# Performance work log

Measured on AMD Instinct MI355X. Metric: run time of the kernel, lower is better.

Reference implementation:

```python
import jax, jax.numpy as jnp
import numpy as np

B, S, D = 4, 2048, 512
QKD = 256
HID = 3 * D  # expansion_factor=3
EPS = 1e-5


def _ln(x, g, b):
    m = jnp.mean(x, axis=-1, keepdims=True)
    v = jnp.mean((x - m) ** 2, axis=-1, keepdims=True)
    return (x - m) * jax.lax.rsqrt(v + EPS) * g + b


def setup_inputs() -> dict:
    key = jax.random.key(0)
    ks = jax.random.split(key, 12)
    s = lambda fan: 1.0 / np.sqrt(fan)
    return {
        "x":  jax.random.normal(ks[0], (B, S, D), jnp.float32),
        "Wm": jax.random.uniform(ks[1], (D, D), jnp.float32, -s(D), s(D)),
        "bm": jnp.zeros((D,), jnp.float32),
        "g1": jnp.ones((D,), jnp.float32),
        "b1": jnp.zeros((D,), jnp.float32),
        "Wh": jax.random.uniform(ks[2], (2 * HID, D), jnp.float32, -s(D), s(D)),
        "bh": jnp.zeros((2 * HID,), jnp.float32),
        "Wq": jax.random.uniform(ks[3], (QKD, D), jnp.float32, -s(D), s(D)),
        "bq": jnp.zeros((QKD,), jnp.float32),
        "Wb": jax.random.normal(ks[4], (QKD, QKD), jnp.float32),
        "Wo": jax.random.uniform(ks[5], (D, HID), jnp.float32, -s(HID), s(HID)),
        "bo": jnp.zeros((D,), jnp.float32),
        "g2": jnp.ones((D,), jnp.float32),
        "b2": jnp.zeros((D,), jnp.float32),
    }


def reference(x, Wm, bm, g1, b1, Wh, bh, Wq, bq, Wb, Wo, bo, g2, b2):
    seq_len = x.shape[-2]
    memory = jnp.einsum('bsd,ed->bse', x, Wm) + bm
    normed = _ln(x + memory, g1, b1)
    h = jax.nn.relu(jnp.einsum('bsd,hd->bsh', normed, Wh) + bh)
    v, gate = h[..., :HID], h[..., HID:]
    Z = jax.nn.relu(jnp.einsum('bsd,qd->bsq', normed, Wq) + bq)  # [B,S,QKD]
    QK = jnp.einsum('bid,de,bje->bij', Z, Wb, Z) / seq_len
    A = jax.nn.relu(QK) ** 2  # relu^2 attention, no softmax
    V = jnp.einsum('bij,bjd->bid', A, v) * gate
    out = _ln(jnp.einsum('bsh,dh->bsd', V, Wo) + bo, g2, b2)
    return out + x
```

## Files before the change

kernel.cpp:

```cpp
#include <hip/hip_runtime.h>

typedef unsigned short u16;
typedef unsigned char u8;
typedef __attribute__((ext_vector_type(8))) short short8;
typedef __attribute__((ext_vector_type(4))) float f32x4;
typedef __attribute__((ext_vector_type(8))) int int8v;
typedef __attribute__((ext_vector_type(4))) int int4v;

#define LN_EPS 1e-5f
#define SCALE_A 4096.f
#define SCALE_V 8.f
#define INV_SCALE_AV (1.f/32768.f)
#define SCALE_NRM 4.f
#define SCALE_WH 512.f
#define INV_SCALE_H (1.f/2048.f)
#define MX_ONE 0x7F7F7F7Fu

__device__ __forceinline__ u16 f2bf(float f){
    union { float f; unsigned u; } c; c.f = f;
    unsigned u = c.u + 0x7FFFu + ((c.u >> 16) & 1u);
    return (u16)(u >> 16);
}
__device__ __forceinline__ float bf2f(u16 h){
    union { unsigned u; float f; } c; c.u = ((unsigned)h) << 16;
    return c.f;
}
__device__ __forceinline__ u8 f2fp8(float f){
    int r = __builtin_amdgcn_cvt_pk_fp8_f32(f, 0.f, 0, false);
    return (u8)(r & 0xFF);
}
__device__ __forceinline__ u16 f2fp8x2(float a, float b){
    int r = __builtin_amdgcn_cvt_pk_fp8_f32(a, b, 0, false);
    return (u16)(r & 0xFFFF);
}

enum { EPI_NONE=0, EPI_BIAS_RES, EPI_BIAS_RELU, EPI_RELUSQ };
enum { OT_F32=0, OT_BF16=1, OT_FP8=2 };

__device__ __forceinline__ void gl2lds16(const void* g, void* lds){
    __builtin_amdgcn_global_load_lds(
        (const __attribute__((address_space(1))) unsigned*)g,
        (__attribute__((address_space(3))) unsigned*)lds, 16, 0, 0);
}

template<int EPI, int OT>
__global__ __launch_bounds__(256)
void mgemm(const u16* __restrict__ A, const u16* __restrict__ B, void* __restrict__ Cv,
           int K, int lda, int ldb, int ldc,
           long sAb, long sBb, long sCb,
           const float* __restrict__ bias,
           const float* __restrict__ ext, int ldext,
           float scale)
{
    __shared__ u16 sA[4096];
    __shared__ u16 sB[4096];
    const int tid = threadIdx.x;
    const int m0 = blockIdx.y * 128, n0 = blockIdx.x * 128;
    const int z  = blockIdx.z;
    const u16* Az = A + (size_t)z * sAb;
    const u16* Bz = B + (size_t)z * sBb;

    const int lane = tid & 63, quad = lane >> 4, l15 = lane & 15;
    const int wave = tid >> 6;
    const int wm = (wave >> 1) * 64, wn = (wave & 1) * 64;

    const u16* gA[2]; const u16* gB[2]; int lo[2];
#pragma unroll
    for (int r = 0; r < 2; r++){
        const int c = tid + r * 256;
        gA[r] = Az + (size_t)(m0 + (c & 127)) * lda + (c >> 7) * 8;
        gB[r] = Bz + (size_t)(n0 + (c & 127)) * ldb + (c >> 7) * 8;
        lo[r] = ((tid & 192) + r * 256) * 16;
    }

    f32x4 acc[4][4];
#pragma unroll
    for (int i = 0; i < 4; i++)
#pragma unroll
        for (int j = 0; j < 4; j++) acc[i][j] = (f32x4){0.f,0.f,0.f,0.f};

    const u16* fA = sA + quad * 1024 + (wm + l15) * 8;
    const u16* fB = sB + quad * 1024 + (wn + l15) * 8;

    for (int k0 = 0; k0 < K; k0 += 32){
#pragma unroll
        for (int r = 0; r < 2; r++){
            gl2lds16(gA[r] + k0, (char*)sA + lo[r]);
            gl2lds16(gB[r] + k0, (char*)sB + lo[r]);
        }
        __syncthreads();
        short8 a[4], b[4];
#pragma unroll
        for (int t = 0; t < 4; t++){
            a[t] = *(const short8*)(fA + t * 128);
            b[t] = *(const short8*)(fB + t * 128);
        }
#pragma unroll
        for (int i = 0; i < 4; i++)
#pragma unroll
            for (int j = 0; j < 4; j++)
                acc[i][j] = __builtin_amdgcn_mfma_f32_16x16x32_bf16(a[i], b[j], acc[i][j], 0, 0, 0);
        __syncthreads();
    }

    float* Cf = (float*)Cv; u16* Ch = (u16*)Cv; u8* C8 = (u8*)Cv;
    const size_t zc = (size_t)z * sCb;
#pragma unroll
    for (int i = 0; i < 4; i++){
#pragma unroll
        for (int j = 0; j < 4; j++){
            const int n = n0 + wn + j * 16 + l15;
            float bs = (EPI==EPI_BIAS_RES || EPI==EPI_BIAS_RELU) ? bias[n] : 0.f;
#pragma unroll
            for (int r = 0; r < 4; r++){
                const int m = m0 + wm + i * 16 + quad * 4 + r;
                float v = acc[i][j][r] + bs;
                if (EPI==EPI_BIAS_RES)
                    v += ext[(size_t)m * ldext + n];
                if (EPI==EPI_BIAS_RELU)
                    v = fmaxf(v, 0.f);
                if (EPI==EPI_RELUSQ){ float t = fmaxf(v * scale, 0.f); v = t * t * SCALE_A; }
                if (OT==OT_FP8)       C8[zc + (size_t)m * ldc + n] = f2fp8(v);
                else if (OT==OT_BF16) Ch[zc + (size_t)m * ldc + n] = f2bf(v);
                else                  Cf[zc + (size_t)m * ldc + n] = v;
            }
        }
    }
}

__global__ __launch_bounds__(256)
void mgemm_dual(const u16* __restrict__ Anrm, const u16* __restrict__ Whg,
                const u16* __restrict__ Wq,
                const float* __restrict__ bhg, const float* __restrict__ bq,
                u16* __restrict__ gbf, u16* __restrict__ Zb)
{
    __shared__ u16 sA[4096];
    __shared__ u16 sB[4096];
    const int tid = threadIdx.x;
    const bool isZ = blockIdx.x >= 12;
    const u16* Bm = isZ ? Wq : Whg;
    const float* bias = isZ ? bq : bhg;
    const int m0 = blockIdx.y * 128;
    const int n0 = (isZ ? (blockIdx.x - 12) : blockIdx.x) * 128;
    const int K = 512, lda = 512, ldb = 512;

    const int lane = tid & 63, quad = lane >> 4, l15 = lane & 15;
    const int wave = tid >> 6;
    const int wm = (wave >> 1) * 64, wn = (wave & 1) * 64;

    const u16* gA[2]; const u16* gB[2]; int lo[2];
#pragma unroll
    for (int r = 0; r < 2; r++){
        const int c = tid + r * 256;
        gA[r] = Anrm + (size_t)(m0 + (c & 127)) * lda + (c >> 7) * 8;
        gB[r] = Bm   + (size_t)(n0 + (c & 127)) * ldb + (c >> 7) * 8;
        lo[r] = ((tid & 192) + r * 256) * 16;
    }

    f32x4 acc[4][4];
#pragma unroll
    for (int i = 0; i < 4; i++)
#pragma unroll
        for (int j = 0; j < 4; j++) acc[i][j] = (f32x4){0.f,0.f,0.f,0.f};

    const u16* fA = sA + quad * 1024 + (wm + l15) * 8;
    const u16* fB = sB + quad * 1024 + (wn + l15) * 8;

    for (int k0 = 0; k0 < K; k0 += 32){
#pragma unroll
        for (int r = 0; r < 2; r++){
            gl2lds16(gA[r] + k0, (char*)sA + lo[r]);
            gl2lds16(gB[r] + k0, (char*)sB + lo[r]);
        }
        __syncthreads();
        short8 a[4], b[4];
#pragma unroll
        for (int t = 0; t < 4; t++){
            a[t] = *(const short8*)(fA + t * 128);
            b[t] = *(const short8*)(fB + t * 128);
        }
#pragma unroll
        for (int i = 0; i < 4; i++)
#pragma unroll
            for (int j = 0; j < 4; j++)
                acc[i][j] = __builtin_amdgcn_mfma_f32_16x16x32_bf16(a[i], b[j], acc[i][j], 0, 0, 0);
        __syncthreads();
    }

#pragma unroll
    for (int i = 0; i < 4; i++){
#pragma unroll
        for (int j = 0; j < 4; j++){
            const int n = n0 + wn + j * 16 + l15;
            const float bs = bias[n];
#pragma unroll
            for (int r = 0; r < 4; r++){
                const int m = m0 + wm + i * 16 + quad * 4 + r;
                float v = fmaxf(acc[i][j][r] + bs, 0.f);
                if (isZ) Zb[(size_t)m * 256 + n] = f2bf(v);
                else     gbf[(size_t)m * 1536 + n] = f2bf(v);
            }
        }
    }
}

template<bool VOUT>
__global__ __launch_bounds__(256)
void mgemm8mx(const u8* __restrict__ A, const u8* __restrict__ B, u16* __restrict__ C,
              int K, int lda, int ldb, int ldc,
              long sAb, long sBb, long sCb,
              const u16* __restrict__ gate, int ldext, long sEb,
              const float* __restrict__ bias, u8* __restrict__ vout)
{
    __shared__ u8 sA[16384];
    __shared__ u8 sB[16384];
    const int tid = threadIdx.x;
    const int m0 = blockIdx.y * 128, n0 = blockIdx.x * 128;
    const int z  = blockIdx.z;
    const u8* Az = A + (size_t)z * sAb;
    const u8* Bz = B + (size_t)z * sBb;

    const int lane = tid & 63, quad = lane >> 4, l15 = lane & 15;
    const int wave = tid >> 6;
    const int wm = (wave >> 1) * 64, wn = (wave & 1) * 64;

    const u8* gA[4]; const u8* gB[4]; int lo[4];
#pragma unroll
    for (int p = 0; p < 4; p++){
        const int r = p * 32 + (tid >> 3);
        const int j = (tid & 7) ^ (r & 7);
        gA[p] = Az + (size_t)(m0 + r) * lda + j * 16;
        gB[p] = Bz + (size_t)(n0 + r) * ldb + j * 16;
        lo[p] = p * 4096 + wave * 1024;
    }

    f32x4 acc[4][4];
#pragma unroll
    for (int i = 0; i < 4; i++)
#pragma unroll
        for (int j = 0; j < 4; j++) acc[i][j] = (f32x4){0.f,0.f,0.f,0.f};

    for (int k0 = 0; k0 < K; k0 += 128){
#pragma unroll
        for (int p = 0; p < 4; p++){
            gl2lds16(gA[p] + k0, (char*)sA + lo[p]);
            gl2lds16(gB[p] + k0, (char*)sB + lo[p]);
        }
        __syncthreads();
        int8v a[4], b[4];
#pragma unroll
        for (int i = 0; i < 4; i++){
            const int m = wm + i * 16 + l15;
            const int4v a0 = *(const int4v*)(sA + m * 128 + ((2*quad    ) ^ (m & 7)) * 16);
            const int4v a1 = *(const int4v*)(sA + m * 128 + ((2*quad + 1) ^ (m & 7)) * 16);
            a[i] = (int8v){a0[0],a0[1],a0[2],a0[3],a1[0],a1[1],a1[2],a1[3]};
            const int n = wn + i * 16 + l15;
            const int4v b0 = *(const int4v*)(sB + n * 128 + ((2*quad    ) ^ (n & 7)) * 16);
            const int4v b1 = *(const int4v*)(sB + n * 128 + ((2*quad + 1) ^ (n & 7)) * 16);
            b[i] = (int8v){b0[0],b0[1],b0[2],b0[3],b1[0],b1[1],b1[2],b1[3]};
        }
#pragma unroll
        for (int i = 0; i < 4; i++)
#pragma unroll
            for (int j = 0; j < 4; j++)
                acc[i][j] = __builtin_amdgcn_mfma_scale_f32_16x16x128_f8f6f4(
                    a[i], b[j], acc[i][j], 0, 0, 0, MX_ONE, 0, MX_ONE);
        __syncthreads();
    }

    const size_t zc = (size_t)z * sCb;
#pragma unroll
    for (int i = 0; i < 4; i++){
#pragma unroll
        for (int j = 0; j < 4; j++){
            const int n = n0 + wn + j * 16 + l15;
#pragma unroll
            for (int r = 0; r < 4; r++){
                const int m = m0 + wm + i * 16 + quad * 4 + r;
                if (VOUT){
                    float h = fmaxf(acc[i][j][r] * INV_SCALE_H + bias[n], 0.f);
                    vout[(size_t)m * 1536 + n] = f2fp8(h * SCALE_V);
                } else {
                    float v = acc[i][j][r] * INV_SCALE_AV
                            * bf2f(gate[(size_t)z * sEb + (size_t)m * ldext + n]);
                    C[zc + (size_t)m * ldc + n] = f2bf(v);
                }
            }
        }
    }
}

__global__ __launch_bounds__(256)
void ln1_k(const float* __restrict__ in, const float* __restrict__ g,
           const float* __restrict__ b, u16* __restrict__ nbf, u16* __restrict__ n8)
{
    const int row = blockIdx.x, tid = threadIdx.x;
    const size_t base = (size_t)row * 512 + tid * 2;
    const float2 v = *(const float2*)(in + base);
    float s = v.x + v.y, ss = v.x * v.x + v.y * v.y;
#pragma unroll
    for (int off = 32; off > 0; off >>= 1){
        s  += __shfl_down(s,  off);
        ss += __shfl_down(ss, off);
    }
    __shared__ float sbuf[8], ssbuf[8];
    const int wid = tid >> 6, lane = tid & 63;
    if (lane == 0){ sbuf[wid] = s; ssbuf[wid] = ss; }
    __syncthreads();
    if (tid == 0){
        float S = 0.f, SS = 0.f;
#pragma unroll
        for (int i = 0; i < 4; i++){ S += sbuf[i]; SS += ssbuf[i]; }
        const float mean = S * (1.f/512.f);
        const float var  = SS * (1.f/512.f) - mean * mean;
        sbuf[4]  = mean;
        ssbuf[4] = rsqrtf(var + LN_EPS);
    }
    __syncthreads();
    const float mean = sbuf[4], rstd = ssbuf[4];
    const float2 gg = *(const float2*)(g + tid * 2);
    const float2 bb = *(const float2*)(b + tid * 2);
    const float ox = (v.x - mean) * rstd * gg.x + bb.x;
    const float oy = (v.y - mean) * rstd * gg.y + bb.y;
    ((unsigned*)nbf)[(size_t)row * 256 + tid] =
        ((unsigned)f2bf(oy) << 16) | (unsigned)f2bf(ox);
    n8[(size_t)row * 256 + tid] = f2fp8x2(ox * SCALE_NRM, oy * SCALE_NRM);
}

__global__ __launch_bounds__(256)
void ln2_k(const u16* __restrict__ pa, long pstride,
           const float* __restrict__ bias2,
           const float* __restrict__ g, const float* __restrict__ b,
           const float* __restrict__ x, float* __restrict__ out)
{
    const int row = blockIdx.x, tid = threadIdx.x;
    const size_t base = (size_t)row * 512 + tid * 2;
    const unsigned p0 = ((const unsigned*)pa)[(size_t)row * 256 + tid];
    const unsigned p1 = ((const unsigned*)(pa + pstride))[(size_t)row * 256 + tid];
    const float2 bb2 = *(const float2*)(bias2 + tid * 2);
    float2 v;
    v.x = bf2f((u16)p0) + bf2f((u16)p1) + bb2.x;
    v.y = bf2f((u16)(p0 >> 16)) + bf2f((u16)(p1 >> 16)) + bb2.y;
    float s = v.x + v.y, ss = v.x * v.x + v.y * v.y;
#pragma unroll
    for (int off = 32; off > 0; off >>= 1){
        s  += __shfl_down(s,  off);
        ss += __shfl_down(ss, off);
    }
    __shared__ float sbuf[8], ssbuf[8];
    const int wid = tid >> 6, lane = tid & 63;
    if (lane == 0){ sbuf[wid] = s; ssbuf[wid] = ss; }
    __syncthreads();
    if (tid == 0){
        float S = 0.f, SS = 0.f;
#pragma unroll
        for (int i = 0; i < 4; i++){ S += sbuf[i]; SS += ssbuf[i]; }
        const float mean = S * (1.f/512.f);
        const float var  = SS * (1.f/512.f) - mean * mean;
        sbuf[4]  = mean;
        ssbuf[4] = rsqrtf(var + LN_EPS);
    }
    __syncthreads();
    const float mean = sbuf[4], rstd = ssbuf[4];
    const float2 gg = *(const float2*)(g + tid * 2);
    const float2 bb = *(const float2*)(b + tid * 2);
    const float2 r = *(const float2*)(x + base);
    float2 o;
    o.x = (v.x - mean) * rstd * gg.x + bb.x + r.x;
    o.y = (v.y - mean) * rstd * gg.y + bb.y + r.y;
    *(float2*)(out + base) = o;
}

__global__ __launch_bounds__(256)
void castall_k(const float* __restrict__ x, const float* __restrict__ Wm,
               const float* __restrict__ Wh, const float* __restrict__ Wq,
               const float* __restrict__ Wo, const float* __restrict__ Wb,
               u16* __restrict__ xb, u16* __restrict__ Wmb, u8* __restrict__ Wh8,
               u16* __restrict__ Whgb,
               u16* __restrict__ Wqb, u16* __restrict__ Wob, u16* __restrict__ WbT)
{
    const int i = blockIdx.x * 256 + threadIdx.x;
    if (i >= 1736704){
        const int j = i - 1736704;
        if (j < 65536){
            const int e = j >> 8, d = j & 255;
            WbT[e * 256 + d] = f2bf(Wb[d * 256 + e]);
        }
        return;
    }
    if (i >= 1114112 && i < 1310720){
        const int off = i - 1114112;
        const float4 v = ((const float4*)Wh)[off];
        unsigned r0 = (unsigned)f2fp8x2(v.x * SCALE_WH, v.y * SCALE_WH);
        unsigned r1 = (unsigned)f2fp8x2(v.z * SCALE_WH, v.w * SCALE_WH);
        ((unsigned*)Wh8)[off] = r0 | (r1 << 16);
        return;
    }
    const float* src; u16* dst; int off;
    if      (i < 1048576){ src = x;  dst = xb;   off = i; }
    else if (i < 1114112){ src = Wm; dst = Wmb;  off = i - 1048576; }
    else if (i < 1507328){ src = Wh + 786432; dst = Whgb; off = i - 1310720; }
    else if (i < 1540096){ src = Wq; dst = Wqb;  off = i - 1507328; }
    else                 { src = Wo; dst = Wob;  off = i - 1540096; }
    const float4 v = ((const float4*)src)[off];
    ushort4 o; o.x = f2bf(v.x); o.y = f2bf(v.y); o.z = f2bf(v.z); o.w = f2bf(v.w);
    ((ushort4*)dst)[off] = o;
}

__global__ __launch_bounds__(256)
void tr8_k(const u8* __restrict__ v, u8* __restrict__ vT, int S, int HID){
    const int b = blockIdx.z;
    const int h0 = blockIdx.x * 64, s0 = blockIdx.y * 64;
    __shared__ u8 t[64][68];
    const u8* vb = v + (size_t)b * S * HID;
    u8* vTb = vT + (size_t)b * HID * S;
    const int tid = threadIdx.x;
#pragma unroll
    for (int i = 0; i < 4; i++){
        int idx = tid + i * 256;
        int r = idx >> 4, c4 = (idx & 15) * 4;
        uchar4 u = *(const uchar4*)(vb + (size_t)(s0 + r) * HID + h0 + c4);
        t[r][c4] = u.x; t[r][c4+1] = u.y; t[r][c4+2] = u.z; t[r][c4+3] = u.w;
    }
    __syncthreads();
#pragma unroll
    for (int i = 0; i < 4; i++){
        int idx = tid + i * 256;
        int r = idx >> 4, c4 = (idx & 15) * 4;
        uchar4 u;
        u.x = t[c4][r]; u.y = t[c4+1][r]; u.z = t[c4+2][r]; u.w = t[c4+3][r];
        *(uchar4*)(vTb + (size_t)(h0 + r) * S + s0 + c4) = u;
    }
}

extern "C" void kernel_launch(void* const* d_in, const int* in_sizes, int n_in,
                              void* d_out, int out_size, void* d_ws, size_t ws_size,
                              hipStream_t stream)
{
    const float* x  = (const float*)d_in[0];
    const float* Wm = (const float*)d_in[1];
    const float* bm = (const float*)d_in[2];
    const float* g1 = (const float*)d_in[3];
    const float* b1 = (const float*)d_in[4];
    const float* Wh = (const float*)d_in[5];
    const float* bh = (const float*)d_in[6];
    const float* Wq = (const float*)d_in[7];
    const float* bq = (const float*)d_in[8];
    const float* Wb = (const float*)d_in[9];
    const float* Wo = (const float*)d_in[10];
    const float* bo = (const float*)d_in[11];
    const float* g2 = (const float*)d_in[12];
    const float* b2 = (const float*)d_in[13];
    float* out = (float*)d_out;
    (void)in_sizes; (void)n_in; (void)out_size; (void)ws_size;

    const int Bn=4, S=2048, D=512, QKD=256, HID=1536;
    const int M = Bn * S;
    const long MD = (long)M * D;

    char* p = (char*)d_ws;
    auto alloc = [&](size_t bytes)->void*{ void* r = p; p += (bytes + 255) & ~(size_t)255; return r; };
    u16*  xbf  = (u16*) alloc((size_t)M*D*2);
    u16*  Wmbf = (u16*) alloc((size_t)D*D*2);
    u8*   Wh8  = (u8*)  alloc((size_t)HID*D);
    u16*  Whgb = (u16*) alloc((size_t)HID*D*2);
    u16*  Wqbf = (u16*) alloc((size_t)QKD*D*2);
    u16*  Wobf = (u16*) alloc((size_t)D*HID*2);
    u16*  WbT  = (u16*) alloc((size_t)QKD*QKD*2);
    float* ybuf= (float*)alloc((size_t)MD*4);
    u16*  wop  = (u16*) alloc((size_t)MD*2*2);
    u16*  n8   = (u16*) alloc((size_t)M*D);
    u16*  Zb   = (u16*) alloc((size_t)M*QKD*2);
    u16*  ZWbb = (u16*) alloc((size_t)M*QKD*2);
    u8*   v8   = (u8*)  alloc((size_t)M*HID);
    u16*  gbf  = (u16*) alloc((size_t)M*HID*2);
    u8*   vT8  = (u8*)  alloc((size_t)M*HID);
    u8*   A8   = (u8*)  alloc((size_t)M*S);
    u16*  Vgbf = (u16*) alloc((size_t)M*HID*2);
    u16*  nrm  = xbf;

    dim3 blk(256);

    castall_k<<<dim3(7040), blk, 0, stream>>>(x, Wm, Wh, Wq, Wo, Wb,
                                              xbf, Wmbf, Wh8, Whgb, Wqbf, Wobf, WbT);
    mgemm<EPI_BIAS_RES,OT_F32><<<dim3(D/128, M/128, 1), blk, 0, stream>>>(
        xbf, Wmbf, ybuf, D, D, D, D, 0,0,0, bm, x, D, 1.f);
    ln1_k<<<dim3(M), blk, 0, stream>>>(ybuf, g1, b1, nrm, n8);
    mgemm8mx<true><<<dim3(HID/128, M/128, 1), blk, 0, stream>>>(
        (const u8*)n8, Wh8, nullptr, D, D, D, 0, 0,0,0,
        nullptr, 0, 0, bh, v8);
    mgemm_dual<<<dim3(14, M/128), blk, 0, stream>>>(
        nrm, Whgb, Wqbf, bh + HID, bq, gbf, Zb);
    mgemm<EPI_NONE,OT_BF16><<<dim3(QKD/128, M/128, 1), blk, 0, stream>>>(
        Zb, WbT, ZWbb, QKD, QKD, QKD, QKD, 0,0,0, nullptr, nullptr, 0, 1.f);
    mgemm<EPI_RELUSQ,OT_FP8><<<dim3(S/128, S/128, Bn), blk, 0, stream>>>(
        ZWbb, Zb, A8, QKD, QKD, QKD, S,
        (long)S*QKD, (long)S*QKD, (long)S*S,
        nullptr, nullptr, 0, 1.f/(float)S);
    tr8_k<<<dim3(HID/64, S/64, Bn), blk, 0, stream>>>(v8, vT8, S, HID);
    mgemm8mx<false><<<dim3(HID/128, S/128, Bn), blk, 0, stream>>>(
        A8, vT8, Vgbf, S, S, S, HID,
        (long)S*S, (long)HID*S, (long)S*HID,
        gbf, HID, (long)S*HID, nullptr, nullptr);
    mgemm<EPI_NONE,OT_BF16><<<dim3(D/128, M/128, 2), blk, 0, stream>>>(
        Vgbf, Wobf, wop, HID/2, HID, HID, D, 768, 768, MD,
        nullptr, nullptr, 0, 1.f);
    ln2_k<<<dim3(M), blk, 0, stream>>>(wop, MD, bo, g2, b2, x, out);
}
```

Before: 312.7 us.

## Merge GEMM launches into combined kernels and split-K the memory and output GEMMs

Merges the fp8 value GEMM, the gate GEMM and the Z GEMM into one launch (dual3_k), and merges the attention-score GEMM with the v transpose into another (batch6_k). This cuts the number of launches and fills more CUs per launch. The memory GEMM now uses split-K with two bf16 partials, which ln1 sums together with the bias and residual. The output GEMM goes from two to four split-K partials, which ln2 sums. This adds bf16 rounding on the partials and more partial-buffer traffic in exchange for more parallelism, and the combined kernels mix work of different lengths in one grid.

```diff
diff --git a/kernel.cpp b/kernel.cpp
--- a/kernel.cpp
+++ b/kernel.cpp
@@ -44,6 +44,82 @@
 }
 
 template<int EPI, int OT>
+__device__ __forceinline__ void bf16_gemm_body(
+    u16* sA, u16* sB,
+    const u16* Az, const u16* Bz, void* Cv,
+    int K, int lda, int ldb, int ldc, size_t zc,
+    int m0, int n0,
+    const float* bias, const float* ext, int ldext, float scale,
+    u16* out_alt, int alt_ld)
+{
+    const int tid = threadIdx.x;
+    const int lane = tid & 63, quad = lane >> 4, l15 = lane & 15;
+    const int wave = tid >> 6;
+    const int wm = (wave >> 1) * 64, wn = (wave & 1) * 64;
+
+    const u16* gA[2]; const u16* gB[2]; int lo[2];
+#pragma unroll
+    for (int r = 0; r < 2; r++){
+        const int c = tid + r * 256;
+        gA[r] = Az + (size_t)(m0 + (c & 127)) * lda + (c >> 7) * 8;
+        gB[r] = Bz + (size_t)(n0 + (c & 127)) * ldb + (c >> 7) * 8;
+        lo[r] = ((tid & 192) + r * 256) * 16;
+    }
+
+    f32x4 acc[4][4];
+#pragma unroll
+    for (int i = 0; i < 4; i++)
+#pragma unroll
+        for (int j = 0; j < 4; j++) acc[i][j] = (f32x4){0.f,0.f,0.f,0.f};
+
+    const u16* fA = sA + quad * 1024 + (wm + l15) * 8;
+    const u16* fB = sB + quad * 1024 + (wn + l15) * 8;
+
+    for (int k0 = 0; k0 < K; k0 += 32){
+#pragma unroll
+        for (int r = 0; r < 2; r++){
+            gl2lds16(gA[r] + k0, (char*)sA + lo[r]);
+            gl2lds16(gB[r] + k0, (char*)sB + lo[r]);
+        }
+        __syncthreads();
+        short8 a[4], b[4];
+#pragma unroll
+        for (int t = 0; t < 4; t++){
+            a[t] = *(const short8*)(fA + t * 128);
+            b[t] = *(const short8*)(fB + t * 128);
+        }
+#pragma unroll
+        for (int i = 0; i < 4; i++)
+#pragma unroll
+            for (int j = 0; j < 4; j++)
+                acc[i][j] = __builtin_amdgcn_mfma_f32_16x16x32_bf16(a[i], b[j], acc[i][j], 0, 0, 0);
+        __syncthreads();
+    }
+
+    float* Cf = (float*)Cv; u16* Ch = (u16*)Cv; u8* C8 = (u8*)Cv;
+#pragma unroll
+    for (int i = 0; i < 4; i++){
+#pragma unroll
+        for (int j = 0; j < 4; j++){
+            const int n = n0 + wn + j * 16 + l15;
+            float bs = (EPI==EPI_BIAS_RES || EPI==EPI_BIAS_RELU) ? bias[n] : 0.f;
+#pragma unroll
+            for (int r = 0; r < 4; r++){
+                const int m = m0 + wm + i * 16 + quad * 4 + r;
+                float v = acc[i][j][r] + bs;
+                if (EPI==EPI_BIAS_RES) v += ext[(size_t)m * ldext + n];
+                if (EPI==EPI_BIAS_RELU) v = fmaxf(v, 0.f);
+                if (EPI==EPI_RELUSQ){ float t = fmaxf(v * scale, 0.f); v = t * t * SCALE_A; }
+                if (OT==OT_FP8)       C8[zc + (size_t)m * ldc + n] = f2fp8(v);
+                else if (OT==OT_BF16) Ch[zc + (size_t)m * ldc + n] = f2bf(v);
+                else                  Cf[zc + (size_t)m * ldc + n] = v;
+            }
+        }
+    }
+    (void)out_alt; (void)alt_ld;
+}
+
+template<int EPI, int OT>
 __global__ __launch_bounds__(256)
 void mgemm(const u16* __restrict__ A, const u16* __restrict__ B, void* __restrict__ Cv,
            int K, int lda, int ldb, int ldc,
@@ -54,172 +130,24 @@
 {
     __shared__ u16 sA[4096];
     __shared__ u16 sB[4096];
+    const int z = blockIdx.z;
+    bf16_gemm_body<EPI,OT>(sA, sB,
+        A + (size_t)z * sAb, B + (size_t)z * sBb, Cv,
+        K, lda, ldb, ldc, (size_t)z * sCb,
+        blockIdx.y * 128, blockIdx.x * 128,
+        bias, ext, ldext, scale, nullptr, 0);
+}
+
+template<bool VOUT>
+__device__ __forceinline__ void mx_gemm_body(
+    u8* sA, u8* sB,
+    const u8* Az, const u8* Bz, u16* C,
+    int K, int lda, int ldb, int ldc, size_t zc,
+    int m0, int n0,
+    const u16* gate, int ldext, size_t ze,
+    const float* bias, u8* vout)
+{
     const int tid = threadIdx.x;
-    const int m0 = blockIdx.y * 128, n0 = blockIdx.x * 128;
-    const int z  = blockIdx.z;
-    const u16* Az = A + (size_t)z * sAb;
-    const u16* Bz = B + (size_t)z * sBb;
-
-    const int lane = tid & 63, quad = lane >> 4, l15 = lane & 15;
-    const int wave = tid >> 6;
-    const int wm = (wave >> 1) * 64, wn = (wave & 1) * 64;
-
-    const u16* gA[2]; const u16* gB[2]; int lo[2];
-#pragma unroll
-    for (int r = 0; r < 2; r++){
-        const int c = tid + r * 256;
-        gA[r] = Az + (size_t)(m0 + (c & 127)) * lda + (c >> 7) * 8;
-        gB[r] = Bz + (size_t)(n0 + (c & 127)) * ldb + (c >> 7) * 8;
-        lo[r] = ((tid & 192) + r * 256) * 16;
-    }
-
-    f32x4 acc[4][4];
-#pragma unroll
-    for (int i = 0; i < 4; i++)
-#pragma unroll
-        for (int j = 0; j < 4; j++) acc[i][j] = (f32x4){0.f,0.f,0.f,0.f};
-
-    const u16* fA = sA + quad * 1024 + (wm + l15) * 8;
-    const u16* fB = sB + quad * 1024 + (wn + l15) * 8;
-
-    for (int k0 = 0; k0 < K; k0 += 32){
-#pragma unroll
-        for (int r = 0; r < 2; r++){
-            gl2lds16(gA[r] + k0, (char*)sA + lo[r]);
-            gl2lds16(gB[r] + k0, (char*)sB + lo[r]);
-        }
-        __syncthreads();
-        short8 a[4], b[4];
-#pragma unroll
-        for (int t = 0; t < 4; t++){
-            a[t] = *(const short8*)(fA + t * 128);
-            b[t] = *(const short8*)(fB + t * 128);
-        }
-#pragma unroll
-        for (int i = 0; i < 4; i++)
-#pragma unroll
-            for (int j = 0; j < 4; j++)
-                acc[i][j] = __builtin_amdgcn_mfma_f32_16x16x32_bf16(a[i], b[j], acc[i][j], 0, 0, 0);
-        __syncthreads();
-    }
-
-    float* Cf = (float*)Cv; u16* Ch = (u16*)Cv; u8* C8 = (u8*)Cv;
-    const size_t zc = (size_t)z * sCb;
-#pragma unroll
-    for (int i = 0; i < 4; i++){
-#pragma unroll
-        for (int j = 0; j < 4; j++){
-            const int n = n0 + wn + j * 16 + l15;
-            float bs = (EPI==EPI_BIAS_RES || EPI==EPI_BIAS_RELU) ? bias[n] : 0.f;
-#pragma unroll
-            for (int r = 0; r < 4; r++){
-                const int m = m0 + wm + i * 16 + quad * 4 + r;
-                float v = acc[i][j][r] + bs;
-                if (EPI==EPI_BIAS_RES)
-                    v += ext[(size_t)m * ldext + n];
-                if (EPI==EPI_BIAS_RELU)
-                    v = fmaxf(v, 0.f);
-                if (EPI==EPI_RELUSQ){ float t = fmaxf(v * scale, 0.f); v = t * t * SCALE_A; }
-                if (OT==OT_FP8)       C8[zc + (size_t)m * ldc + n] = f2fp8(v);
-                else if (OT==OT_BF16) Ch[zc + (size_t)m * ldc + n] = f2bf(v);
-                else                  Cf[zc + (size_t)m * ldc + n] = v;
-            }
-        }
-    }
-}
-
-__global__ __launch_bounds__(256)
-void mgemm_dual(const u16* __restrict__ Anrm, const u16* __restrict__ Whg,
-                const u16* __restrict__ Wq,
-                const float* __restrict__ bhg, const float* __restrict__ bq,
-                u16* __restrict__ gbf, u16* __restrict__ Zb)
-{
-    __shared__ u16 sA[4096];
-    __shared__ u16 sB[4096];
-    const int tid = threadIdx.x;
-    const bool isZ = blockIdx.x >= 12;
-    const u16* Bm = isZ ? Wq : Whg;
-    const float* bias = isZ ? bq : bhg;
-    const int m0 = blockIdx.y * 128;
-    const int n0 = (isZ ? (blockIdx.x - 12) : blockIdx.x) * 128;
-    const int K = 512, lda = 512, ldb = 512;
-
-    const int lane = tid & 63, quad = lane >> 4, l15 = lane & 15;
-    const int wave = tid >> 6;
-    const int wm = (wave >> 1) * 64, wn = (wave & 1) * 64;
-
-    const u16* gA[2]; const u16* gB[2]; int lo[2];
-#pragma unroll
-    for (int r = 0; r < 2; r++){
-        const int c = tid + r * 256;
-        gA[r] = Anrm + (size_t)(m0 + (c & 127)) * lda + (c >> 7) * 8;
-        gB[r] = Bm   + (size_t)(n0 + (c & 127)) * ldb + (c >> 7) * 8;
-        lo[r] = ((tid & 192) + r * 256) * 16;
-    }
-
-    f32x4 acc[4][4];
-#pragma unroll
-    for (int i = 0; i < 4; i++)
-#pragma unroll
-        for (int j = 0; j < 4; j++) acc[i][j] = (f32x4){0.f,0.f,0.f,0.f};
-
-    const u16* fA = sA + quad * 1024 + (wm + l15) * 8;
-    const u16* fB = sB + quad * 1024 + (wn + l15) * 8;
-
-    for (int k0 = 0; k0 < K; k0 += 32){
-#pragma unroll
-        for (int r = 0; r < 2; r++){
-            gl2lds16(gA[r] + k0, (char*)sA + lo[r]);
-            gl2lds16(gB[r] + k0, (char*)sB + lo[r]);
-        }
-        __syncthreads();
-        short8 a[4], b[4];
-#pragma unroll
-        for (int t = 0; t < 4; t++){
-            a[t] = *(const short8*)(fA + t * 128);
-            b[t] = *(const short8*)(fB + t * 128);
-        }
-#pragma unroll
-        for (int i = 0; i < 4; i++)
-#pragma unroll
-            for (int j = 0; j < 4; j++)
-                acc[i][j] = __builtin_amdgcn_mfma_f32_16x16x32_bf16(a[i], b[j], acc[i][j], 0, 0, 0);
-        __syncthreads();
-    }
-
-#pragma unroll
-    for (int i = 0; i < 4; i++){
-#pragma unroll
-        for (int j = 0; j < 4; j++){
-            const int n = n0 + wn + j * 16 + l15;
-            const float bs = bias[n];
-#pragma unroll
-            for (int r = 0; r < 4; r++){
-                const int m = m0 + wm + i * 16 + quad * 4 + r;
-                float v = fmaxf(acc[i][j][r] + bs, 0.f);
-                if (isZ) Zb[(size_t)m * 256 + n] = f2bf(v);
-                else     gbf[(size_t)m * 1536 + n] = f2bf(v);
-            }
-        }
-    }
-}
-
-template<bool VOUT>
-__global__ __launch_bounds__(256)
-void mgemm8mx(const u8* __restrict__ A, const u8* __restrict__ B, u16* __restrict__ C,
-              int K, int lda, int ldb, int ldc,
-              long sAb, long sBb, long sCb,
-              const u16* __restrict__ gate, int ldext, long sEb,
-              const float* __restrict__ bias, u8* __restrict__ vout)
-{
-    __shared__ u8 sA[16384];
-    __shared__ u8 sB[16384];
-    const int tid = threadIdx.x;
-    const int m0 = blockIdx.y * 128, n0 = blockIdx.x * 128;
-    const int z  = blockIdx.z;
-    const u8* Az = A + (size_t)z * sAb;
-    const u8* Bz = B + (size_t)z * sBb;
-
     const int lane = tid & 63, quad = lane >> 4, l15 = lane & 15;
     const int wave = tid >> 6;
     const int wm = (wave >> 1) * 64, wn = (wave & 1) * 64;
@@ -268,7 +196,6 @@
         __syncthreads();
     }
 
-    const size_t zc = (size_t)z * sCb;
 #pragma unroll
     for (int i = 0; i < 4; i++){
 #pragma unroll
@@ -282,7 +209,7 @@
                     vout[(size_t)m * 1536 + n] = f2fp8(h * SCALE_V);
                 } else {
                     float v = acc[i][j][r] * INV_SCALE_AV
-                            * bf2f(gate[(size_t)z * sEb + (size_t)m * ldext + n]);
+                            * bf2f(gate[ze + (size_t)m * ldext + n]);
                     C[zc + (size_t)m * ldc + n] = f2bf(v);
                 }
             }
@@ -291,12 +218,108 @@
 }
 
 __global__ __launch_bounds__(256)
-void ln1_k(const float* __restrict__ in, const float* __restrict__ g,
-           const float* __restrict__ b, u16* __restrict__ nbf, u16* __restrict__ n8)
+void mgemm8mx(const u8* __restrict__ A, const u8* __restrict__ B, u16* __restrict__ C,
+              int K, int lda, int ldb, int ldc,
+              long sAb, long sBb, long sCb,
+              const u16* __restrict__ gate, int ldext, long sEb)
+{
+    __shared__ u8 sA[16384];
+    __shared__ u8 sB[16384];
+    const int z = blockIdx.z;
+    mx_gemm_body<false>(sA, sB,
+        A + (size_t)z * sAb, B + (size_t)z * sBb, C,
+        K, lda, ldb, ldc, (size_t)z * sCb,
+        blockIdx.y * 128, blockIdx.x * 128,
+        gate, ldext, (size_t)z * sEb, nullptr, nullptr);
+}
+
+__global__ __launch_bounds__(256)
+void dual3_k(const u16* __restrict__ nrm, const u16* __restrict__ n8,
+             const u8* __restrict__ Wh8, const u16* __restrict__ Whgb,
+             const u16* __restrict__ Wqbf,
+             const float* __restrict__ bh, const float* __restrict__ bq,
+             u8* __restrict__ v8, u16* __restrict__ gbf, u16* __restrict__ Zb)
+{
+    __shared__ char lds[32768];
+    const int bx = blockIdx.x;
+    const int m0 = blockIdx.y * 128;
+    if (bx < 12){
+        mx_gemm_body<true>((u8*)lds, (u8*)lds + 16384,
+            (const u8*)n8, Wh8, nullptr,
+            512, 512, 512, 0, 0,
+            m0, bx * 128,
+            nullptr, 0, 0, bh, v8);
+    } else if (bx < 24){
+        bf16_gemm_body<EPI_BIAS_RELU,OT_BF16>((u16*)lds, (u16*)lds + 4096,
+            nrm, Whgb, gbf,
+            512, 512, 512, 1536, 0,
+            m0, (bx - 12) * 128,
+            bh + 1536, nullptr, 0, 1.f, nullptr, 0);
+    } else {
+        bf16_gemm_body<EPI_BIAS_RELU,OT_BF16>((u16*)lds, (u16*)lds + 4096,
+            nrm, Wqbf, Zb,
+            512, 512, 512, 256, 0,
+            m0, (bx - 24) * 128,
+            bq, nullptr, 0, 1.f, nullptr, 0);
+    }
+}
+
+__global__ __launch_bounds__(256)
+void batch6_k(const u16* __restrict__ ZWbb, const u16* __restrict__ Zb,
+              u8* __restrict__ A8,
+              const u8* __restrict__ v8, u8* __restrict__ vT8)
+{
+    __shared__ char lds[16384];
+    const int bx = blockIdx.x;
+    const int z  = blockIdx.y;
+    const int S = 2048, QKD = 256, HID = 1536;
+    if (bx < 256){
+        bf16_gemm_body<EPI_RELUSQ,OT_FP8>((u16*)lds, (u16*)lds + 4096,
+            ZWbb + (size_t)z * S * QKD, Zb + (size_t)z * S * QKD, A8,
+            QKD, QKD, QKD, S, (size_t)z * S * S,
+            (bx >> 4) * 128, (bx & 15) * 128,
+            nullptr, nullptr, 0, 1.f/(float)S, nullptr, 0);
+    } else {
+        const int idx = bx - 256;
+        const int h0 = (idx % 24) * 64, s0 = (idx / 24) * 64;
+        u8 (*t)[68] = (u8(*)[68])lds;
+        const u8* vb = v8 + (size_t)z * S * HID;
+        u8* vTb = vT8 + (size_t)z * HID * S;
+        const int tid = threadIdx.x;
+#pragma unroll
+        for (int i = 0; i < 4; i++){
+            int id2 = tid + i * 256;
+            int r = id2 >> 4, c4 = (id2 & 15) * 4;
+            uchar4 u = *(const uchar4*)(vb + (size_t)(s0 + r) * HID + h0 + c4);
+            t[r][c4] = u.x; t[r][c4+1] = u.y; t[r][c4+2] = u.z; t[r][c4+3] = u.w;
+        }
+        __syncthreads();
+#pragma unroll
+        for (int i = 0; i < 4; i++){
+            int id2 = tid + i * 256;
+            int r = id2 >> 4, c4 = (id2 & 15) * 4;
+            uchar4 u;
+            u.x = t[c4][r]; u.y = t[c4+1][r]; u.z = t[c4+2][r]; u.w = t[c4+3][r];
+            *(uchar4*)(vTb + (size_t)(h0 + r) * S + s0 + c4) = u;
+        }
+    }
+}
+
+__global__ __launch_bounds__(256)
+void ln1_k(const u16* __restrict__ pa, long pstride,
+           const float* __restrict__ bm, const float* __restrict__ x,
+           const float* __restrict__ g, const float* __restrict__ b,
+           u16* __restrict__ nbf, u16* __restrict__ n8)
 {
     const int row = blockIdx.x, tid = threadIdx.x;
     const size_t base = (size_t)row * 512 + tid * 2;
-    const float2 v = *(const float2*)(in + base);
+    const unsigned p0 = ((const unsigned*)pa)[(size_t)row * 256 + tid];
+    const unsigned p1 = ((const unsigned*)(pa + pstride))[(size_t)row * 256 + tid];
+    const float2 bb0 = *(const float2*)(bm + tid * 2);
+    const float2 xx  = *(const float2*)(x + base);
+    float2 v;
+    v.x = bf2f((u16)p0) + bf2f((u16)p1) + bb0.x + xx.x;
+    v.y = bf2f((u16)(p0 >> 16)) + bf2f((u16)(p1 >> 16)) + bb0.y + xx.y;
     float s = v.x + v.y, ss = v.x * v.x + v.y * v.y;
 #pragma unroll
     for (int off = 32; off > 0; off >>= 1){
@@ -335,12 +358,14 @@
 {
     const int row = blockIdx.x, tid = threadIdx.x;
     const size_t base = (size_t)row * 512 + tid * 2;
-    const unsigned p0 = ((const unsigned*)pa)[(size_t)row * 256 + tid];
-    const unsigned p1 = ((const unsigned*)(pa + pstride))[(size_t)row * 256 + tid];
     const float2 bb2 = *(const float2*)(bias2 + tid * 2);
-    float2 v;
-    v.x = bf2f((u16)p0) + bf2f((u16)p1) + bb2.x;
-    v.y = bf2f((u16)(p0 >> 16)) + bf2f((u16)(p1 >> 16)) + bb2.y;
+    float2 v = make_float2(bb2.x, bb2.y);
+#pragma unroll
+    for (int p = 0; p < 4; p++){
+        const unsigned pk = ((const unsigned*)(pa + (size_t)p * pstride))[(size_t)row * 256 + tid];
+        v.x += bf2f((u16)pk);
+        v.y += bf2f((u16)(pk >> 16));
+    }
     float s = v.x + v.y, ss = v.x * v.x + v.y * v.y;
 #pragma unroll
     for (int off = 32; off > 0; off >>= 1){
@@ -405,32 +430,6 @@
     const float4 v = ((const float4*)src)[off];
     ushort4 o; o.x = f2bf(v.x); o.y = f2bf(v.y); o.z = f2bf(v.z); o.w = f2bf(v.w);
     ((ushort4*)dst)[off] = o;
-}
-
-__global__ __launch_bounds__(256)
-void tr8_k(const u8* __restrict__ v, u8* __restrict__ vT, int S, int HID){
-    const int b = blockIdx.z;
-    const int h0 = blockIdx.x * 64, s0 = blockIdx.y * 64;
-    __shared__ u8 t[64][68];
-    const u8* vb = v + (size_t)b * S * HID;
-    u8* vTb = vT + (size_t)b * HID * S;
-    const int tid = threadIdx.x;
-#pragma unroll
-    for (int i = 0; i < 4; i++){
-        int idx = tid + i * 256;
-        int r = idx >> 4, c4 = (idx & 15) * 4;
-        uchar4 u = *(const uchar4*)(vb + (size_t)(s0 + r) * HID + h0 + c4);
-        t[r][c4] = u.x; t[r][c4+1] = u.y; t[r][c4+2] = u.z; t[r][c4+3] = u.w;
-    }
-    __syncthreads();
-#pragma unroll
-    for (int i = 0; i < 4; i++){
-        int idx = tid + i * 256;
-        int r = idx >> 4, c4 = (idx & 15) * 4;
-        uchar4 u;
-        u.x = t[c4][r]; u.y = t[c4+1][r]; u.z = t[c4+2][r]; u.w = t[c4+3][r];
-        *(uchar4*)(vTb + (size_t)(h0 + r) * S + s0 + c4) = u;
-    }
 }
 
 extern "C" void kernel_launch(void* const* d_in, const int* in_sizes, int n_in,
@@ -467,8 +466,7 @@
     u16*  Wqbf = (u16*) alloc((size_t)QKD*D*2);
     u16*  Wobf = (u16*) alloc((size_t)D*HID*2);
     u16*  WbT  = (u16*) alloc((size_t)QKD*QKD*2);
-    float* ybuf= (float*)alloc((size_t)MD*4);
-    u16*  wop  = (u16*) alloc((size_t)MD*2*2);
+    u16*  wop  = (u16*) alloc((size_t)MD*2*4);
     u16*  n8   = (u16*) alloc((size_t)M*D);
     u16*  Zb   = (u16*) alloc((size_t)M*QKD*2);
     u16*  ZWbb = (u16*) alloc((size_t)M*QKD*2);
@@ -483,27 +481,21 @@
 
     castall_k<<<dim3(7040), blk, 0, stream>>>(x, Wm, Wh, Wq, Wo, Wb,
                                               xbf, Wmbf, Wh8, Whgb, Wqbf, Wobf, WbT);
-    mgemm<EPI_BIAS_RES,OT_F32><<<dim3(D/128, M/128, 1), blk, 0, stream>>>(
-        xbf, Wmbf, ybuf, D, D, D, D, 0,0,0, bm, x, D, 1.f);
-    ln1_k<<<dim3(M), blk, 0, stream>>>(ybuf, g1, b1, nrm, n8);
-    mgemm8mx<true><<<dim3(HID/128, M/128, 1), blk, 0, stream>>>(
-        (const u8*)n8, Wh8, nullptr, D, D, D, 0, 0,0,0,
-        nullptr, 0, 0, bh, v8);
-    mgemm_dual<<<dim3(14, M/128), blk, 0, stream>>>(
-        nrm, Whgb, Wqbf, bh + HID, bq, gbf, Zb);
+    mgemm<EPI_NONE,OT_BF16><<<dim3(D/128, M/128, 2), blk, 0, stream>>>(
+        xbf, Wmbf, wop, D/2, D, D, D, 256, 256, MD,
+        nullptr, nullptr, 0, 1.f);
+    ln1_k<<<dim3(M), blk, 0, stream>>>(wop, MD, bm, x, g1, b1, nrm, n8);
+    dual3_k<<<dim3(26, M/128), blk, 0, stream>>>(
+        nrm, n8, Wh8, Whgb, Wqbf, bh, bq, v8, gbf, Zb);
     mgemm<EPI_NONE,OT_BF16><<<dim3(QKD/128, M/128, 1), blk, 0, stream>>>(
         Zb, WbT, ZWbb, QKD, QKD, QKD, QKD, 0,0,0, nullptr, nullptr, 0, 1.f);
-    mgemm<EPI_RELUSQ,OT_FP8><<<dim3(S/128, S/128, Bn), blk, 0, stream>>>(
-        ZWbb, Zb, A8, QKD, QKD, QKD, S,
-        (long)S*QKD, (long)S*QKD, (long)S*S,
-        nullptr, nullptr, 0, 1.f/(float)S);
-    tr8_k<<<dim3(HID/64, S/64, Bn), blk, 0, stream>>>(v8, vT8, S, HID);
-    mgemm8mx<false><<<dim3(HID/128, S/128, Bn), blk, 0, stream>>>(
+    batch6_k<<<dim3(1024, Bn), blk, 0, stream>>>(ZWbb, Zb, A8, v8, vT8);
+    mgemm8mx<<<dim3(HID/128, S/128, Bn), blk, 0, stream>>>(
         A8, vT8, Vgbf, S, S, S, HID,
         (long)S*S, (long)HID*S, (long)S*HID,
-        gbf, HID, (long)S*HID, nullptr, nullptr);
-    mgemm<EPI_NONE,OT_BF16><<<dim3(D/128, M/128, 2), blk, 0, stream>>>(
-        Vgbf, Wobf, wop, HID/2, HID, HID, D, 768, 768, MD,
+        gbf, HID, (long)S*HID);
+    mgemm<EPI_NONE,OT_BF16><<<dim3(D/128, M/128, 4), blk, 0, stream>>>(
+        Vgbf, Wobf, wop, HID/4, HID, HID, D, 384, 384, MD,
         nullptr, nullptr, 0, 1.f);
     ln2_k<<<dim3(M), blk, 0, stream>>>(wop, MD, bo, g2, b2, x, out);
 }
```

Result: slower. 323.9 us (+3.6%).
